# Kernel optimization log

Hardware: AMD Instinct MI355X
Metric: run time of the kernel (lower is better)

## Reference

```python
import jax, jax.numpy as jnp
import numpy as np

N_PTS = 131072
IN_CH = 63
IN_CH_VIEWS = 27
WIDTH = 256
NUM_HEADS = 4
SCALE = 0.05


def setup_inputs() -> dict:
    key = jax.random.key(0)
    ks = jax.random.split(key, 12)
    H, W = NUM_HEADS, WIDTH
    inp = {
        'x': jax.random.normal(ks[0], (N_PTS, IN_CH + IN_CH_VIEWS), jnp.float32),
        'head_idx': jax.random.randint(ks[1], (N_PTS,), 0, NUM_HEADS),
        # shared trunk: layer0 63->256, layers1..3 256->256 (no skip before split_at=4)
        'W0': jax.random.normal(ks[2], (IN_CH, W), jnp.float32) * SCALE,
        'b0': jnp.zeros((W,), jnp.float32),
        'Ws': jax.random.normal(ks[3], (3, W, W), jnp.float32) * SCALE,
        'bs': jnp.zeros((3, W), jnp.float32),
        # per-head tails: g=4 in skips -> (W+63)->W, then g=5..7 W->W
        'tW0': jax.random.normal(ks[4], (H, W + IN_CH, W), jnp.float32) * SCALE,
        'tb0': jnp.zeros((H, W), jnp.float32),
        'tWs': jax.random.normal(ks[5], (H, 3, W, W), jnp.float32) * SCALE,
        'tbs': jnp.zeros((H, 3, W), jnp.float32),
        # per-head viewdirs output heads
        'featW': jax.random.normal(ks[6], (H, W, W), jnp.float32) * SCALE,
        'featb': jnp.zeros((H, W), jnp.float32),
        'alphaW': jax.random.normal(ks[7], (H, W, 1), jnp.float32) * SCALE,
        'alphab': jnp.zeros((H, 1), jnp.float32),
        'viewsW': jax.random.normal(ks[8], (H, IN_CH_VIEWS + W, W // 2), jnp.float32) * SCALE,
        'viewsb': jnp.zeros((H, W // 2), jnp.float32),
        'rgbW': jax.random.normal(ks[9], (H, W // 2, 3), jnp.float32) * SCALE,
        'rgbb': jnp.zeros((H, 3), jnp.float32),
    }
    return inp


def reference(x, head_idx, W0, b0, Ws, bs, tW0, tb0, tWs, tbs,
              featW, featb, alphaW, alphab, viewsW, viewsb, rgbW, rgbb):
    input_pts = x[:, :IN_CH]          # [N, 63]
    input_views = x[:, IN_CH:]        # [N, 27]

    # shared trunk (layers 0..3, no skip hits in this range)
    h = jax.nn.relu(input_pts @ W0 + b0)
    for i in range(Ws.shape[0]):
        h = jax.nn.relu(h @ Ws[i] + bs[i])

    # per-head tails, computed densely for ALL heads (as in the original)
    # first tail layer g=4 is a skip layer: concat input_pts
    ht = jnp.concatenate([input_pts, h], axis=-1)          # [N, 319]
    ha = jax.nn.relu(jnp.einsum('nf,hfo->nho', ht, tW0) + tb0[None])  # [N, H, 256]
    for j in range(tWs.shape[1]):
        ha = jax.nn.relu(jnp.einsum('nho,hop->nhp', ha, tWs[:, j]) + tbs[None, :, j])

    # per-head viewdir output heads
    alpha = jnp.einsum('nho,hop->nhp', ha, alphaW) + alphab[None]     # [N, H, 1]
    feat = jnp.einsum('nho,hop->nhp', ha, featW) + featb[None]        # [N, H, 256]
    views_b = jnp.broadcast_to(input_views[:, None, :], (x.shape[0], feat.shape[1], IN_CH_VIEWS))
    hv = jnp.concatenate([feat, views_b], axis=-1)                    # [N, H, 283]
    hv = jax.nn.relu(jnp.einsum('nho,hop->nhp', hv, viewsW) + viewsb[None])
    rgb = jnp.einsum('nho,hop->nhp', hv, rgbW) + rgbb[None]           # [N, H, 3]

    outs = jnp.concatenate([rgb, alpha], axis=-1)                     # [N, H, 4]
    sel = jnp.take_along_axis(outs, head_idx[:, None, None], axis=1)[:, 0]  # [N, 4]
    return sel
```

## Files before the change

### kernel.cpp

```cpp
#include <hip/hip_runtime.h>

#define N_PTS 131072
#define TILE 64
#define THREADS 512

typedef __bf16 bf16;
typedef __bf16 bf16x8 __attribute__((ext_vector_type(8)));
typedef float f32x4 __attribute__((ext_vector_type(4)));

#define WS_PERM_OFF   256
#define WS_WPACK_OFF  (256 + N_PTS * 4)
#define OFF_W0     0
#define OFF_WS     16384
#define OFF_TW0    212992
#define OFF_TWS    540672
#define OFF_FEATW  1327104
#define OFF_VIEWSW 1589248
#define TOTAL_PACK 1736704

#define PTS_BASE 0
#define H_BASE   8192
#define B_BASE   40960
#define LDS_BYTES 73728

__device__ __forceinline__ unsigned swz(unsigned base, unsigned row, unsigned rowstride,
                                        unsigned kbyte) {
  return (base + row * rowstride + kbyte) ^ ((row & 7u) << 4);
}

__device__ __forceinline__ void gload_lds16(const bf16* g, char* l) {
  __builtin_amdgcn_global_load_lds(
      (const __attribute__((address_space(1))) void*)g,
      (__attribute__((address_space(3))) void*)l, 16, 0, 0);
}

__global__ void k_pack(const float* __restrict__ W0, const float* __restrict__ Ws,
                       const float* __restrict__ tW0, const float* __restrict__ tWs,
                       const float* __restrict__ featW, const float* __restrict__ viewsW,
                       bf16* __restrict__ out, const int* __restrict__ head,
                       int* __restrict__ ctrl) {
  __shared__ int lc[4];
  if (threadIdx.x < 4) lc[threadIdx.x] = 0;
  __syncthreads();
  int gid = blockIdx.x * blockDim.x + threadIdx.x;
  if (gid < N_PTS) atomicAdd(&lc[head[gid]], 1);

  for (int idx = gid; idx < TOTAL_PACK; idx += gridDim.x * blockDim.x) {
    float v;
    if (idx < OFF_WS) {
      int o = idx >> 6, k = idx & 63;
      v = (k < 63) ? W0[k * 256 + o] : 0.f;
    } else if (idx < OFF_TW0) {
      int i = idx - OFF_WS; int l = i >> 16, r = i & 65535, o = r >> 8, k = r & 255;
      v = Ws[l * 65536 + k * 256 + o];
    } else if (idx < OFF_TWS) {
      int i = idx - OFF_TW0; int h = i / 81920, r = i % 81920, o = r / 320, k = r % 320;
      v = (k < 63) ? tW0[(h * 319 + k) * 256 + o]
                   : (k == 63 ? 0.f : tW0[(h * 319 + k - 1) * 256 + o]);
    } else if (idx < OFF_FEATW) {
      int i = idx - OFF_TWS; int hj = i >> 16, r = i & 65535, o = r >> 8, k = r & 255;
      v = tWs[(hj * 256 + k) * 256 + o];
    } else if (idx < OFF_VIEWSW) {
      int i = idx - OFF_FEATW; int h = i >> 16, r = i & 65535, o = r >> 8, k = r & 255;
      v = featW[(h * 256 + k) * 256 + o];
    } else {
      int i = idx - OFF_VIEWSW; int h = i / 36864, r = i % 36864, o = r / 288, k = r % 288;
      v = (k < 283) ? viewsW[(h * 283 + k) * 128 + o] : 0.f;
    }
    out[idx] = (bf16)v;
  }
  __syncthreads();
  if (threadIdx.x < 4 && lc[threadIdx.x]) atomicAdd(&ctrl[threadIdx.x], lc[threadIdx.x]);
}

__global__ void k_scan(int* c) {
  c[8] = 0; c[24] = 0;
  for (int h = 0; h < 4; ++h) {
    c[8 + h + 1] = c[8 + h] + c[h];
    c[16 + h] = c[8 + h];
    c[24 + h + 1] = c[24 + h] + (c[h] + TILE - 1) / TILE;
  }
}

__global__ void k_scatter(const int* __restrict__ head, int* __restrict__ c,
                          int* __restrict__ perm) {
  int p = blockIdx.x * 256 + threadIdx.x;
  int h = (p < N_PTS) ? head[p] : -1;
  int lane = threadIdx.x & 63;
  #pragma unroll
  for (int hh = 0; hh < 4; ++hh) {
    unsigned long long m = __ballot(h == hh);
    if (m == 0ull) continue;
    int leader = __builtin_ctzll(m);
    int base = 0;
    if (lane == leader) base = atomicAdd(&c[16 + hh], __popcll(m));
    base = __shfl(base, leader);
    if (h == hh) {
      int rank = __popcll(m & ((1ull << lane) - 1ull));
      perm[base + rank] = p;
    }
  }
}

template <int OUTS>
__device__ __forceinline__ void stage_B(const bf16* __restrict__ Wt, int wK, int kk,
                                        char* lds, int bufsel, int wave, int lane) {
  constexpr int ISSUES = OUTS / 128;
  #pragma unroll
  for (int s = 0; s < ISSUES; ++s) {
    int reg = wave * ISSUES + s;
    int o = reg * 16 + (lane >> 2);
    int j = lane & 3;
    const bf16* g = Wt + o * wK + kk + ((j ^ ((o >> 1) & 3)) << 3);
    gload_lds16(g, lds + B_BASE + bufsel * 16384 + reg * 1024);
  }
}

template <int MR, int NF, bool RELU, int A0KC, int A1KC, int OUTS>
__device__ __forceinline__ void mfma_layer(char* lds, const bf16* __restrict__ Wt, int wK,
                                           const float* __restrict__ bias,
                                           int a0_base, int a0_stride,
                                           int a1_base, int a1_stride,
                                           int out_base, int out_stride,
                                           int lane, int wave) {
  const int l15 = lane & 15, l4 = lane >> 4;
  const int wr = wave >> 2, wc = wave & 3;
  constexpr int KC = A0KC + A1KC;
  f32x4 acc[MR][NF];
  #pragma unroll
  for (int m = 0; m < MR; ++m)
    #pragma unroll
    for (int n = 0; n < NF; ++n) acc[m][n] = (f32x4){0.f, 0.f, 0.f, 0.f};

  const int r0 = wr * (MR * 16);
  const int c0 = wc * (NF * 16);

  stage_B<OUTS>(Wt, wK, 0, lds, 0, wave, lane);

  #pragma unroll 1
  for (int kc = 0; kc < KC; ++kc) {
    asm volatile("s_waitcnt vmcnt(0)" ::: "memory");
    __builtin_amdgcn_s_barrier();

    const int buf = kc & 1;
    if (kc + 1 < KC) stage_B<OUTS>(Wt, wK, (kc + 1) * 32, lds, buf ^ 1, wave, lane);

    const int base   = (kc < A0KC) ? a0_base   : a1_base;
    const int stride = (kc < A0KC) ? a0_stride : a1_stride;
    const int kl     = ((kc < A0KC) ? kc : kc - A0KC) * 32;
    bf16x8 a[MR];
    #pragma unroll
    for (int m = 0; m < MR; ++m)
      a[m] = *(const bf16x8*)(lds + swz(base, r0 + m * 16 + l15, stride,
                                        (kl + l4 * 8) * 2));
    bf16x8 b[NF];
    #pragma unroll
    for (int n = 0; n < NF; ++n) {
      int col = c0 + n * 16 + l15;
      b[n] = *(const bf16x8*)(lds + B_BASE + buf * 16384 + col * 64 +
                              ((l4 ^ ((col >> 1) & 3)) << 4));
    }

    __builtin_amdgcn_s_setprio(1);
    #pragma unroll
    for (int n = 0; n < NF; ++n)
      #pragma unroll
      for (int m = 0; m < MR; ++m)
        acc[m][n] = __builtin_amdgcn_mfma_f32_16x16x32_bf16(a[m], b[n], acc[m][n], 0, 0, 0);
    __builtin_amdgcn_s_setprio(0);
  }

  __builtin_amdgcn_s_barrier();

  #pragma unroll
  for (int n = 0; n < NF; ++n) {
    int col = c0 + n * 16 + l15;
    float bv = bias[col];
    #pragma unroll
    for (int m = 0; m < MR; ++m) {
      #pragma unroll
      for (int j = 0; j < 4; ++j) {
        float v = acc[m][n][j] + bv;
        if (RELU) v = fmaxf(v, 0.f);
        int row = r0 + m * 16 + l4 * 4 + j;
        *(bf16*)(lds + swz(out_base, row, out_stride, col * 2)) = (bf16)v;
      }
    }
  }
  __syncthreads();
}

__global__ __launch_bounds__(THREADS, 4) void k_main(
    const float* __restrict__ x, const int* __restrict__ ctrl, const int* __restrict__ perm,
    const bf16* __restrict__ wpack,
    const float* __restrict__ b0, const float* __restrict__ bs,
    const float* __restrict__ tb0p, const float* __restrict__ tbsp,
    const float* __restrict__ featb, const float* __restrict__ alphaW,
    const float* __restrict__ alphab, const float* __restrict__ viewsb,
    const float* __restrict__ rgbW, const float* __restrict__ rgbb,
    float* __restrict__ outp) {
  __shared__ __attribute__((aligned(16))) char lds[LDS_BYTES];
  __shared__ int pidx[TILE];
  __shared__ float alpha_s[TILE];

  const int tid = threadIdx.x;
  const int lane = tid & 63, wave = tid >> 6;

  const int tbA = ctrl[24], tbB = ctrl[25], tbC = ctrl[26], tbD = ctrl[27], tbE = ctrl[28];
  const int bid = blockIdx.x;
  if (bid >= tbE) return;
  const int hh = (bid >= tbB) + (bid >= tbC) + (bid >= tbD);
  const int tb_h = (hh == 0) ? tbA : ((hh == 1) ? tbB : ((hh == 2) ? tbC : tbD));
  const int start = ctrl[8 + hh] + (bid - tb_h) * TILE;
  const int nv = min(TILE, ctrl[8 + hh + 1] - start);

  if (tid < TILE) pidx[tid] = (tid < nv) ? perm[start + tid] : -1;
  __syncthreads();

  for (int i = tid; i < TILE * 64; i += THREADS) {
    int row = i >> 6, c = i & 63;
    int p = pidx[row];
    float v = (p >= 0 && c < 63) ? x[p * 90 + c] : 0.f;
    *(bf16*)(lds + swz(PTS_BASE, row, 128, c * 2)) = (bf16)v;
  }
  __syncthreads();

  const bf16* W0p    = wpack + OFF_W0;
  const bf16* Wsp    = wpack + OFF_WS;
  const bf16* tW0p   = wpack + OFF_TW0 + hh * 81920;
  const bf16* tWsp   = wpack + OFF_TWS + hh * 3 * 65536;
  const bf16* featWp = wpack + OFF_FEATW + hh * 65536;
  const bf16* viewsWp= wpack + OFF_VIEWSW + hh * 36864;

  mfma_layer<2, 4, true, 2, 0, 256>(lds, W0p, 64, b0, PTS_BASE, 128, 0, 0, H_BASE, 512, lane, wave);
  mfma_layer<2, 4, true, 8, 0, 256>(lds, Wsp,          256, bs,       H_BASE, 512, 0, 0, H_BASE, 512, lane, wave);
  mfma_layer<2, 4, true, 8, 0, 256>(lds, Wsp + 65536,  256, bs + 256, H_BASE, 512, 0, 0, H_BASE, 512, lane, wave);
  mfma_layer<2, 4, true, 8, 0, 256>(lds, Wsp + 131072, 256, bs + 512, H_BASE, 512, 0, 0, H_BASE, 512, lane, wave);
  mfma_layer<2, 4, true, 2, 8, 256>(lds, tW0p, 320, tb0p + hh * 256,
                                    PTS_BASE, 128, H_BASE, 512, H_BASE, 512, lane, wave);

  for (int i = tid; i < TILE * 32; i += THREADS) {
    int row = i >> 5, c = i & 31;
    int p = pidx[row];
    float v = (p >= 0 && c < 27) ? x[p * 90 + 63 + c] : 0.f;
    *(bf16*)(lds + swz(PTS_BASE, row, 128, c * 2)) = (bf16)v;
  }
  __syncthreads();

  mfma_layer<2, 4, true, 8, 0, 256>(lds, tWsp,          256, tbsp + hh * 768,       H_BASE, 512, 0, 0, H_BASE, 512, lane, wave);
  mfma_layer<2, 4, true, 8, 0, 256>(lds, tWsp + 65536,  256, tbsp + hh * 768 + 256, H_BASE, 512, 0, 0, H_BASE, 512, lane, wave);
  mfma_layer<2, 4, true, 8, 0, 256>(lds, tWsp + 131072, 256, tbsp + hh * 768 + 512, H_BASE, 512, 0, 0, H_BASE, 512, lane, wave);

  if (wave < 4) {
    int p = wave * 16 + (lane & 15);
    int kq = lane >> 4;
    const float* aW = alphaW + hh * 256;
    float s = 0.f;
    for (int i = 0; i < 8; ++i) {
      int k = kq * 64 + i * 8;
      bf16x8 hv8 = *(const bf16x8*)(lds + swz(H_BASE, p, 512, k * 2));
      #pragma unroll
      for (int j = 0; j < 8; ++j) s += (float)hv8[j] * aW[k + j];
    }
    s += __shfl_xor(s, 16);
    s += __shfl_xor(s, 32);
    if (kq == 0) alpha_s[p] = s + alphab[hh];
  }

  mfma_layer<2, 4, false, 8, 0, 256>(lds, featWp, 256, featb + hh * 256,
                                     H_BASE, 512, 0, 0, H_BASE, 512, lane, wave);
  mfma_layer<2, 2, true, 8, 1, 128>(lds, viewsWp, 288, viewsb + hh * 128,
                                    H_BASE, 512, PTS_BASE, 128, H_BASE, 512, lane, wave);

  if (wave < 4) {
    int p = wave * 16 + (lane & 15);
    int kq = lane >> 4;
    const float* rW = rgbW + hh * 128 * 3;
    float r0 = 0.f, r1 = 0.f, r2 = 0.f;
    for (int i = 0; i < 4; ++i) {
      int k = kq * 32 + i * 8;
      bf16x8 hv8 = *(const bf16x8*)(lds + swz(H_BASE, p, 512, k * 2));
      #pragma unroll
      for (int j = 0; j < 8; ++j) {
        float hvf = (float)hv8[j];
        r0 += hvf * rW[(k + j) * 3 + 0];
        r1 += hvf * rW[(k + j) * 3 + 1];
        r2 += hvf * rW[(k + j) * 3 + 2];
      }
    }
    r0 += __shfl_xor(r0, 16); r0 += __shfl_xor(r0, 32);
    r1 += __shfl_xor(r1, 16); r1 += __shfl_xor(r1, 32);
    r2 += __shfl_xor(r2, 16); r2 += __shfl_xor(r2, 32);
    if (kq == 0 && p < nv) {
      int pt = pidx[p];
      float4 o = make_float4(r0 + rgbb[hh * 3 + 0], r1 + rgbb[hh * 3 + 1],
                             r2 + rgbb[hh * 3 + 2], alpha_s[p]);
      *(float4*)(outp + pt * 4) = o;
    }
  }
}

extern "C" void kernel_launch(void* const* d_in, const int* in_sizes, int n_in,
                              void* d_out, int out_size, void* d_ws, size_t ws_size,
                              hipStream_t stream) {
  const float* x      = (const float*)d_in[0];
  const int*   head   = (const int*)d_in[1];
  const float* W0     = (const float*)d_in[2];
  const float* b0     = (const float*)d_in[3];
  const float* Ws     = (const float*)d_in[4];
  const float* bs     = (const float*)d_in[5];
  const float* tW0    = (const float*)d_in[6];
  const float* tb0    = (const float*)d_in[7];
  const float* tWs    = (const float*)d_in[8];
  const float* tbs    = (const float*)d_in[9];
  const float* featW  = (const float*)d_in[10];
  const float* featb  = (const float*)d_in[11];
  const float* alphaW = (const float*)d_in[12];
  const float* alphab = (const float*)d_in[13];
  const float* viewsW = (const float*)d_in[14];
  const float* viewsb = (const float*)d_in[15];
  const float* rgbW   = (const float*)d_in[16];
  const float* rgbb   = (const float*)d_in[17];

  int*  ctrl  = (int*)d_ws;
  int*  perm  = (int*)((char*)d_ws + WS_PERM_OFF);
  bf16* wpack = (bf16*)((char*)d_ws + WS_WPACK_OFF);

  hipMemsetAsync(ctrl, 0, 256, stream);
  k_pack<<<2048, 256, 0, stream>>>(W0, Ws, tW0, tWs, featW, viewsW, wpack, head, ctrl);
  k_scan<<<1, 1, 0, stream>>>(ctrl);
  k_scatter<<<N_PTS / 256, 256, 0, stream>>>(head, ctrl, perm);
  k_main<<<N_PTS / TILE + 4, THREADS, 0, stream>>>(x, ctrl, perm, wpack,
                                                   b0, bs, tb0, tbs, featb, alphaW, alphab,
                                                   viewsb, rgbW, rgbb, (float*)d_out);
}
```

Measured before the change: 423.8 us.

## Fold head bucketing into pack kernel with fixed per-head regions; relax launch bounds

```diff
diff --git a/kernel.cpp b/kernel.cpp
--- a/kernel.cpp
+++ b/kernel.cpp
@@ -3,13 +3,14 @@
 #define N_PTS 131072
 #define TILE 64
 #define THREADS 512
+#define REGION 40960
 
 typedef __bf16 bf16;
 typedef __bf16 bf16x8 __attribute__((ext_vector_type(8)));
 typedef float f32x4 __attribute__((ext_vector_type(4)));
 
 #define WS_PERM_OFF   256
-#define WS_WPACK_OFF  (256 + N_PTS * 4)
+#define WS_WPACK_OFF  (256 + 4 * REGION * 4)
 #define OFF_W0     0
 #define OFF_WS     16384
 #define OFF_TW0    212992
@@ -38,12 +39,25 @@
                        const float* __restrict__ tW0, const float* __restrict__ tWs,
                        const float* __restrict__ featW, const float* __restrict__ viewsW,
                        bf16* __restrict__ out, const int* __restrict__ head,
-                       int* __restrict__ ctrl) {
-  __shared__ int lc[4];
-  if (threadIdx.x < 4) lc[threadIdx.x] = 0;
-  __syncthreads();
+                       int* __restrict__ ctrl, int* __restrict__ perm) {
   int gid = blockIdx.x * blockDim.x + threadIdx.x;
-  if (gid < N_PTS) atomicAdd(&lc[head[gid]], 1);
+  if (gid < N_PTS) {
+    int h = head[gid];
+    int lane = threadIdx.x & 63;
+    #pragma unroll
+    for (int hh = 0; hh < 4; ++hh) {
+      unsigned long long m = __ballot(h == hh);
+      if (m == 0ull) continue;
+      int leader = __builtin_ctzll(m);
+      int base = 0;
+      if (lane == leader) base = atomicAdd(&ctrl[16 + hh], __popcll(m));
+      base = __shfl(base, leader);
+      if (h == hh) {
+        int rank = __popcll(m & ((1ull << lane) - 1ull));
+        perm[hh * REGION + base + rank] = gid;
+      }
+    }
+  }
 
   for (int idx = gid; idx < TOTAL_PACK; idx += gridDim.x * blockDim.x) {
     float v;
@@ -69,37 +83,6 @@
     }
     out[idx] = (bf16)v;
   }
-  __syncthreads();
-  if (threadIdx.x < 4 && lc[threadIdx.x]) atomicAdd(&ctrl[threadIdx.x], lc[threadIdx.x]);
-}
-
-__global__ void k_scan(int* c) {
-  c[8] = 0; c[24] = 0;
-  for (int h = 0; h < 4; ++h) {
-    c[8 + h + 1] = c[8 + h] + c[h];
-    c[16 + h] = c[8 + h];
-    c[24 + h + 1] = c[24 + h] + (c[h] + TILE - 1) / TILE;
-  }
-}
-
-__global__ void k_scatter(const int* __restrict__ head, int* __restrict__ c,
-                          int* __restrict__ perm) {
-  int p = blockIdx.x * 256 + threadIdx.x;
-  int h = (p < N_PTS) ? head[p] : -1;
-  int lane = threadIdx.x & 63;
-  #pragma unroll
-  for (int hh = 0; hh < 4; ++hh) {
-    unsigned long long m = __ballot(h == hh);
-    if (m == 0ull) continue;
-    int leader = __builtin_ctzll(m);
-    int base = 0;
-    if (lane == leader) base = atomicAdd(&c[16 + hh], __popcll(m));
-    base = __shfl(base, leader);
-    if (h == hh) {
-      int rank = __popcll(m & ((1ull << lane) - 1ull));
-      perm[base + rank] = p;
-    }
-  }
 }
 
 template <int OUTS>
@@ -190,7 +173,7 @@
   __syncthreads();
 }
 
-__global__ __launch_bounds__(THREADS, 4) void k_main(
+__global__ __launch_bounds__(THREADS, 2) void k_main(
     const float* __restrict__ x, const int* __restrict__ ctrl, const int* __restrict__ perm,
     const bf16* __restrict__ wpack,
     const float* __restrict__ b0, const float* __restrict__ bs,
@@ -206,15 +189,13 @@
   const int tid = threadIdx.x;
   const int lane = tid & 63, wave = tid >> 6;
 
-  const int tbA = ctrl[24], tbB = ctrl[25], tbC = ctrl[26], tbD = ctrl[27], tbE = ctrl[28];
-  const int bid = blockIdx.x;
-  if (bid >= tbE) return;
-  const int hh = (bid >= tbB) + (bid >= tbC) + (bid >= tbD);
-  const int tb_h = (hh == 0) ? tbA : ((hh == 1) ? tbB : ((hh == 2) ? tbC : tbD));
-  const int start = ctrl[8 + hh] + (bid - tb_h) * TILE;
-  const int nv = min(TILE, ctrl[8 + hh + 1] - start);
-
-  if (tid < TILE) pidx[tid] = (tid < nv) ? perm[start + tid] : -1;
+  const int hh = blockIdx.x / (REGION / TILE);
+  const int start = (blockIdx.x % (REGION / TILE)) * TILE;
+  const int cnt = ctrl[16 + hh];
+  if (start >= cnt) return;
+  const int nv = min(TILE, cnt - start);
+
+  if (tid < TILE) pidx[tid] = (tid < nv) ? perm[hh * REGION + start + tid] : -1;
   __syncthreads();
 
   for (int i = tid; i < TILE * 64; i += THREADS) {
@@ -327,10 +308,8 @@
   bf16* wpack = (bf16*)((char*)d_ws + WS_WPACK_OFF);
 
   hipMemsetAsync(ctrl, 0, 256, stream);
-  k_pack<<<2048, 256, 0, stream>>>(W0, Ws, tW0, tWs, featW, viewsW, wpack, head, ctrl);
-  k_scan<<<1, 1, 0, stream>>>(ctrl);
-  k_scatter<<<N_PTS / 256, 256, 0, stream>>>(head, ctrl, perm);
-  k_main<<<N_PTS / TILE + 4, THREADS, 0, stream>>>(x, ctrl, perm, wpack,
-                                                   b0, bs, tb0, tbs, featb, alphaW, alphab,
-                                                   viewsb, rgbW, rgbb, (float*)d_out);
-}
+  k_pack<<<2048, 256, 0, stream>>>(W0, Ws, tW0, tWs, featW, viewsW, wpack, head, ctrl, perm);
+  k_main<<<4 * (REGION / TILE), THREADS, 0, stream>>>(x, ctrl, perm, wpack,
+                                                      b0, bs, tb0, tbs, featb, alphaW, alphab,
+                                                      viewsb, rgbW, rgbb, (float*)d_out);
+}
```

Result: slower. 551.0 us (+30.0%).
